# Kernel optimization log

Measured on AMD Instinct MI355X. Metric: run time of the kernel, lower is better.

The kernel has to match this reference:

```python
import jax, jax.numpy as jnp
import numpy as np

B, T, F, OUT = 32, 8192, 128, 1024

def setup_inputs() -> dict:
    key = jax.random.key(0)
    kx, kl = jax.random.split(key)
    x = jax.random.normal(kx, (B, T, F), dtype=jnp.float32)
    # true (unpadded) lengths; module assumes max(lengths) == T (padded length)
    lengths = jax.random.randint(kl, (B,), OUT + 1, T + 1)
    lengths = lengths.at[0].set(T)
    return {"x": x, "lengths": lengths, "output_size": OUT}

def reference(x, lengths, output_size):
    # Original math: per-sample box filter of length f_b = lengths_b - output_size + 1
    # (ones / f_b, zero-padded to max) applied as grouped conv over time:
    #   out[b, t, f] = (1/f_b) * sum_{k=0}^{f_b-1} x[b, t+k, f],  t in [0, output_size)
    # Implemented via prefix sums instead of materializing the sparse filter bank.
    fsize = lengths - output_size + 1                                  # [B]
    cs = jnp.cumsum(x, axis=1)                                         # [B, T, F]
    cs = jnp.concatenate([jnp.zeros_like(cs[:, :1]), cs], axis=1)      # [B, T+1, F]
    t = jnp.arange(output_size)                                        # [OUT]
    idx = (t[None, :] + fsize[:, None])[:, :, None]                    # [B, OUT, 1]
    hi = jnp.take_along_axis(cs, idx, axis=1)                          # [B, OUT, F]
    lo = cs[:, :output_size, :]                                        # [B, OUT, F]
    return (hi - lo) / fsize[:, None, None].astype(x.dtype)
```

## Files before the change

kernel.cpp:

```cpp
#include <hip/hip_runtime.h>

#define NB    32
#define NT    8192
#define NF    128
#define NOUT  1024
#define NSEG  256
#define NGRP  64
#define TILE  32
#define NTILE (NOUT/TILE)

__device__ __forceinline__ float4 f4add(float4 a, float4 b) {
  return make_float4(a.x + b.x, a.y + b.y, a.z + b.z, a.w + b.w);
}
__device__ __forceinline__ float4 f4sub(float4 a, float4 b) {
  return make_float4(a.x - b.x, a.y - b.y, a.z - b.z, a.w - b.w);
}

__global__ __launch_bounds__(256) void seg_sums(const float* __restrict__ x,
                                                const int* __restrict__ lengths,
                                                float* __restrict__ S32,
                                                float* __restrict__ S128) {
  const int blk = blockIdx.x;
  const int b   = blk >> 6;
  const int g   = blk & 63;
  const int len = lengths[b];
  if (g * 128 >= len) return;

  const int tid = threadIdx.x;
  const int fl  = tid & 31;
  const int tl  = tid >> 5;

  const float4* xp =
      reinterpret_cast<const float4*>(x + (size_t)b * NT * NF +
                                      (size_t)(g * 128) * NF) + fl;
  float4 acc = make_float4(0.f, 0.f, 0.f, 0.f);
  #pragma unroll
  for (int r = 0; r < 16; ++r)
    acc = f4add(acc, xp[(tl * 16 + r) * 32]);

  __shared__ float4 red[8][32];
  red[tl][fl] = acc;
  __syncthreads();
  if (tl < 4) {
    float4 s = f4add(red[2 * tl][fl], red[2 * tl + 1][fl]);
    reinterpret_cast<float4*>(S32 + ((size_t)b * NSEG + g * 4 + tl) * NF)[fl] = s;
  } else if (tl == 4) {
    float4 s = f4add(f4add(red[0][fl], red[1][fl]),
                     f4add(red[2][fl], red[3][fl]));
    s = f4add(s, f4add(f4add(red[4][fl], red[5][fl]),
                       f4add(red[6][fl], red[7][fl])));
    reinterpret_cast<float4*>(S128 + ((size_t)b * NGRP + g) * NF)[fl] = s;
  }
}

__global__ __launch_bounds__(256) void window_avg(const float* __restrict__ x,
                                                  const int* __restrict__ lengths,
                                                  const float* __restrict__ S32,
                                                  const float* __restrict__ S128,
                                                  float* __restrict__ out) {
  const int wg   = ((blockIdx.x & 7) << 7) + (blockIdx.x >> 3);
  const int b    = wg >> 5;
  const int tile = wg & (NTILE - 1);
  const int len  = lengths[b];
  const int W    = len - NOUT + 1;
  const int t0   = tile * TILE;
  const int p1   = t0 + W;
  const int s_hi = p1 >> 5;
  const int g_lo = (t0 + 127) >> 7;
  const int g_hi = p1 >> 7;

  const int tid = threadIdx.x;
  const int fl  = tid & 31;
  const int tl  = tid >> 5;

  const float4* xb =
      reinterpret_cast<const float4*>(x + (size_t)b * NT * NF) + fl;
  const float4* S32b =
      reinterpret_cast<const float4*>(S32 + (size_t)b * NSEG * NF) + fl;
  const float4* S128b =
      reinterpret_cast<const float4*>(S128 + (size_t)b * NGRP * NF) + fl;

  float4 acc = make_float4(0.f, 0.f, 0.f, 0.f);
  if (g_hi > g_lo) {
    for (int s = tile + tl; s < 4 * g_lo; s += 8)
      acc = f4add(acc, S32b[s * 32]);
    for (int g = g_lo + tl; g < g_hi; g += 8)
      acc = f4add(acc, S128b[g * 32]);
    for (int s = 4 * g_hi + tl; s < s_hi; s += 8)
      acc = f4add(acc, S32b[s * 32]);
  } else {
    for (int s = tile + tl; s < s_hi; s += 8)
      acc = f4add(acc, S32b[s * 32]);
  }
  for (int j = (s_hi << 5) + tl; j < p1; j += 8)
    acc = f4add(acc, xb[j * 32]);

  __shared__ float4 red[8][32];
  red[tl][fl] = acc;
  __syncthreads();
  float4 A = make_float4(0.f, 0.f, 0.f, 0.f);
  #pragma unroll
  for (int k = 0; k < 8; ++k) A = f4add(A, red[k][fl]);
  __syncthreads();

  float4 D = make_float4(0.f, 0.f, 0.f, 0.f);
  if (tl < 7) {
    const int baseLo = t0 + 4 * tl;
    const int baseHi = p1 + 4 * tl;
    #pragma unroll
    for (int j = 0; j < 4; ++j) {
      float4 h = xb[(baseHi + j) * 32];
      float4 l = xb[(baseLo + j) * 32];
      D = f4add(D, f4sub(h, l));
    }
  }
  red[tl][fl] = D;
  __syncthreads();
  #pragma unroll
  for (int k = 0; k < 7; ++k)
    if (k < tl) A = f4add(A, red[k][fl]);

  const float invW  = 1.0f / (float)W;
  const int   tbase = t0 + 4 * tl;
  float4* ob =
      reinterpret_cast<float4*>(out + ((size_t)b * NOUT + tbase) * NF) + fl;

  #pragma unroll
  for (int i = 0; i < 4; ++i) {
    ob[i * 32] = make_float4(A.x * invW, A.y * invW, A.z * invW, A.w * invW);
    if (i < 3) {
      float4 h = xb[(tbase + i + W) * 32];
      float4 l = xb[(tbase + i) * 32];
      A = f4add(A, f4sub(h, l));
    }
  }
}

extern "C" void kernel_launch(void* const* d_in, const int* in_sizes, int n_in,
                              void* d_out, int out_size, void* d_ws, size_t ws_size,
                              hipStream_t stream) {
  const float* x       = (const float*)d_in[0];
  const int*   lengths = (const int*)d_in[1];
  float*       S32     = (float*)d_ws;
  float*       S128    = (float*)d_ws + (size_t)NB * NSEG * NF;
  float*       out     = (float*)d_out;

  hipLaunchKernelGGL(seg_sums, dim3(NB * NGRP), dim3(256), 0, stream,
                     x, lengths, S32, S128);
  hipLaunchKernelGGL(window_avg, dim3(NB * NTILE), dim3(256), 0, stream,
                     x, lengths, S32, S128, out);
}
```

Baseline: 29.46 us.

## Fuse segment-sum and window kernels with per-batch atomic completion counters

Merges the two kernel launches into one persistent-style kernel. Each block first computes its segment sums, then signals a per-batch atomic counter. The first 32 blocks per batch spin until all 64 groups of that batch are done and then compute the window averages. This removes one launch and the grid-wide barrier between the stages, so batches can overlap. In exchange it adds a memset launch, a host attribute query on every call, spin-wait latency, and a deadlock risk if the blocks are not all co-resident. A register-count check falls back to the old two-kernel path.

New measurement: 29.74 us. About the same (+0.9%).

```diff
diff --git a/kernel.cpp b/kernel.cpp
--- a/kernel.cpp
+++ b/kernel.cpp
@@ -16,52 +16,39 @@
   return make_float4(a.x - b.x, a.y - b.y, a.z - b.z, a.w - b.w);
 }
 
-__global__ __launch_bounds__(256) void seg_sums(const float* __restrict__ x,
-                                                const int* __restrict__ lengths,
-                                                float* __restrict__ S32,
-                                                float* __restrict__ S128) {
-  const int blk = blockIdx.x;
-  const int b   = blk >> 6;
-  const int g   = blk & 63;
-  const int len = lengths[b];
-  if (g * 128 >= len) return;
-
-  const int tid = threadIdx.x;
-  const int fl  = tid & 31;
-  const int tl  = tid >> 5;
-
-  const float4* xp =
-      reinterpret_cast<const float4*>(x + (size_t)b * NT * NF +
-                                      (size_t)(g * 128) * NF) + fl;
-  float4 acc = make_float4(0.f, 0.f, 0.f, 0.f);
-  #pragma unroll
-  for (int r = 0; r < 16; ++r)
-    acc = f4add(acc, xp[(tl * 16 + r) * 32]);
-
-  __shared__ float4 red[8][32];
-  red[tl][fl] = acc;
-  __syncthreads();
-  if (tl < 4) {
-    float4 s = f4add(red[2 * tl][fl], red[2 * tl + 1][fl]);
-    reinterpret_cast<float4*>(S32 + ((size_t)b * NSEG + g * 4 + tl) * NF)[fl] = s;
-  } else if (tl == 4) {
-    float4 s = f4add(f4add(red[0][fl], red[1][fl]),
-                     f4add(red[2][fl], red[3][fl]));
-    s = f4add(s, f4add(f4add(red[4][fl], red[5][fl]),
-                       f4add(red[6][fl], red[7][fl])));
-    reinterpret_cast<float4*>(S128 + ((size_t)b * NGRP + g) * NF)[fl] = s;
-  }
-}
-
-__global__ __launch_bounds__(256) void window_avg(const float* __restrict__ x,
-                                                  const int* __restrict__ lengths,
-                                                  const float* __restrict__ S32,
-                                                  const float* __restrict__ S128,
-                                                  float* __restrict__ out) {
-  const int wg   = ((blockIdx.x & 7) << 7) + (blockIdx.x >> 3);
-  const int b    = wg >> 5;
-  const int tile = wg & (NTILE - 1);
-  const int len  = lengths[b];
+__device__ __forceinline__ void phase1_group(const float4* __restrict__ xb,
+                                             int b, int g, int len,
+                                             float* __restrict__ S32,
+                                             float* __restrict__ S128,
+                                             int tl, int fl, float4 (*red)[32]) {
+  if (g * 128 < len) {
+    const float4* xp = xb + (size_t)(g * 128) * 32;
+    float4 acc = make_float4(0.f, 0.f, 0.f, 0.f);
+    #pragma unroll
+    for (int r = 0; r < 16; ++r)
+      acc = f4add(acc, xp[(tl * 16 + r) * 32]);
+    red[tl][fl] = acc;
+    __syncthreads();
+    if (tl < 4) {
+      float4 s = f4add(red[2 * tl][fl], red[2 * tl + 1][fl]);
+      reinterpret_cast<float4*>(S32 + ((size_t)b * NSEG + g * 4 + tl) * NF)[fl] = s;
+    } else if (tl == 4) {
+      float4 s = f4add(f4add(red[0][fl], red[1][fl]),
+                       f4add(red[2][fl], red[3][fl]));
+      s = f4add(s, f4add(f4add(red[4][fl], red[5][fl]),
+                         f4add(red[6][fl], red[7][fl])));
+      reinterpret_cast<float4*>(S128 + ((size_t)b * NGRP + g) * NF)[fl] = s;
+    }
+    __syncthreads();
+  }
+}
+
+__device__ __forceinline__ void phase2_tile(const float4* __restrict__ xb,
+                                            int b, int tile, int len,
+                                            const float* __restrict__ S32,
+                                            const float* __restrict__ S128,
+                                            float* __restrict__ out,
+                                            int tl, int fl, float4 (*red)[32]) {
   const int W    = len - NOUT + 1;
   const int t0   = tile * TILE;
   const int p1   = t0 + W;
@@ -69,16 +56,8 @@
   const int g_lo = (t0 + 127) >> 7;
   const int g_hi = p1 >> 7;
 
-  const int tid = threadIdx.x;
-  const int fl  = tid & 31;
-  const int tl  = tid >> 5;
-
-  const float4* xb =
-      reinterpret_cast<const float4*>(x + (size_t)b * NT * NF) + fl;
-  const float4* S32b =
-      reinterpret_cast<const float4*>(S32 + (size_t)b * NSEG * NF) + fl;
-  const float4* S128b =
-      reinterpret_cast<const float4*>(S128 + (size_t)b * NGRP * NF) + fl;
+  const float4* S32b  = reinterpret_cast<const float4*>(S32  + (size_t)b * NSEG * NF) + fl;
+  const float4* S128b = reinterpret_cast<const float4*>(S128 + (size_t)b * NGRP * NF) + fl;
 
   float4 acc = make_float4(0.f, 0.f, 0.f, 0.f);
   if (g_hi > g_lo) {
@@ -95,7 +74,6 @@
   for (int j = (s_hi << 5) + tl; j < p1; j += 8)
     acc = f4add(acc, xb[j * 32]);
 
-  __shared__ float4 red[8][32];
   red[tl][fl] = acc;
   __syncthreads();
   float4 A = make_float4(0.f, 0.f, 0.f, 0.f);
@@ -108,11 +86,8 @@
     const int baseLo = t0 + 4 * tl;
     const int baseHi = p1 + 4 * tl;
     #pragma unroll
-    for (int j = 0; j < 4; ++j) {
-      float4 h = xb[(baseHi + j) * 32];
-      float4 l = xb[(baseLo + j) * 32];
-      D = f4add(D, f4sub(h, l));
-    }
+    for (int j = 0; j < 4; ++j)
+      D = f4add(D, f4sub(xb[(baseHi + j) * 32], xb[(baseLo + j) * 32]));
   }
   red[tl][fl] = D;
   __syncthreads();
@@ -122,8 +97,7 @@
 
   const float invW  = 1.0f / (float)W;
   const int   tbase = t0 + 4 * tl;
-  float4* ob =
-      reinterpret_cast<float4*>(out + ((size_t)b * NOUT + tbase) * NF) + fl;
+  float4* ob = reinterpret_cast<float4*>(out + ((size_t)b * NOUT + tbase) * NF) + fl;
 
   #pragma unroll
   for (int i = 0; i < 4; ++i) {
@@ -136,6 +110,71 @@
   }
 }
 
+__global__ __launch_bounds__(256) void fused_pipe(const float* __restrict__ x,
+                                                  const int* __restrict__ lengths,
+                                                  float* __restrict__ S32,
+                                                  float* __restrict__ S128,
+                                                  unsigned int* __restrict__ done,
+                                                  float* __restrict__ out) {
+  const int bid = blockIdx.x;
+  const int wg  = ((bid & 7) << 8) | (bid >> 3);
+  const int b   = wg >> 6;
+  const int g   = wg & 63;
+  const int len = lengths[b];
+  const int tid = threadIdx.x;
+  const int fl  = tid & 31;
+  const int tl  = tid >> 5;
+
+  __shared__ float4 red[8][32];
+  const float4* xb = reinterpret_cast<const float4*>(x + (size_t)b * NT * NF) + fl;
+
+  phase1_group(xb, b, g, len, S32, S128, tl, fl, red);
+
+  __threadfence();
+  __syncthreads();
+  if (tid == 0)
+    __hip_atomic_fetch_add(&done[b], 1u, __ATOMIC_RELEASE, __HIP_MEMORY_SCOPE_AGENT);
+
+  if (g < NTILE) {
+    if (tid == 0) {
+      while (__hip_atomic_load(&done[b], __ATOMIC_ACQUIRE, __HIP_MEMORY_SCOPE_AGENT)
+             < (unsigned)NGRP)
+        __builtin_amdgcn_s_sleep(8);
+    }
+    __syncthreads();
+    phase2_tile(xb, b, g, len, S32, S128, out, tl, fl, red);
+  }
+}
+
+__global__ __launch_bounds__(256) void k_seg(const float* __restrict__ x,
+                                             const int* __restrict__ lengths,
+                                             float* __restrict__ S32,
+                                             float* __restrict__ S128) {
+  const int blk = blockIdx.x;
+  const int b   = blk >> 6;
+  const int g   = blk & 63;
+  const int len = lengths[b];
+  const int tid = threadIdx.x;
+  __shared__ float4 red[8][32];
+  const float4* xb = reinterpret_cast<const float4*>(x + (size_t)b * NT * NF) + (tid & 31);
+  phase1_group(xb, b, g, len, S32, S128, tid >> 5, tid & 31, red);
+}
+
+__global__ __launch_bounds__(256) void k_win(const float* __restrict__ x,
+                                             const int* __restrict__ lengths,
+                                             const float* __restrict__ S32,
+                                             const float* __restrict__ S128,
+                                             float* __restrict__ out) {
+  const int wg   = ((blockIdx.x & 7) << 7) + (blockIdx.x >> 3);
+  const int b    = wg >> 5;
+  const int tile = wg & (NTILE - 1);
+  const int len  = lengths[b];
+  const int tid  = threadIdx.x;
+  __shared__ float4 red[8][32];
+  const float4* xb = reinterpret_cast<const float4*>(x + (size_t)b * NT * NF) + (tid & 31);
+  phase2_tile(xb, b, tile, len, S32, S128, out, tid >> 5, tid & 31, red);
+}
+
 extern "C" void kernel_launch(void* const* d_in, const int* in_sizes, int n_in,
                               void* d_out, int out_size, void* d_ws, size_t ws_size,
                               hipStream_t stream) {
@@ -143,10 +182,22 @@
   const int*   lengths = (const int*)d_in[1];
   float*       S32     = (float*)d_ws;
   float*       S128    = (float*)d_ws + (size_t)NB * NSEG * NF;
+  unsigned int* done   = (unsigned int*)((float*)d_ws +
+                          (size_t)NB * (NSEG + NGRP) * NF);
   float*       out     = (float*)d_out;
 
-  hipLaunchKernelGGL(seg_sums, dim3(NB * NGRP), dim3(256), 0, stream,
-                     x, lengths, S32, S128);
-  hipLaunchKernelGGL(window_avg, dim3(NB * NTILE), dim3(256), 0, stream,
-                     x, lengths, S32, S128, out);
-}
+  hipFuncAttributes attr{};
+  bool pipe_ok = (hipFuncGetAttributes(&attr, (const void*)fused_pipe) == hipSuccess)
+                 && attr.numRegs <= 64;
+
+  if (pipe_ok) {
+    hipMemsetAsync(done, 0, NB * sizeof(unsigned int), stream);
+    hipLaunchKernelGGL(fused_pipe, dim3(NB * NGRP), dim3(256), 0, stream,
+                       x, lengths, S32, S128, done, out);
+  } else {
+    hipLaunchKernelGGL(k_seg, dim3(NB * NGRP), dim3(256), 0, stream,
+                       x, lengths, S32, S128);
+    hipLaunchKernelGGL(k_win, dim3(NB * NTILE), dim3(256), 0, stream,
+                       x, lengths, S32, S128, out);
+  }
+}
```
